# Performance work log

Hardware: AMD Instinct MI355X
Metric: run time of the kernel (lower is better)

Reference implementation:

```python
import jax, jax.numpy as jnp
import numpy as np

NEG_SLOPE = 0.2


def gat_layer(x, src, dst, W, a_src, a_dst, bias, num_nodes, concat):
    """PyG-style GATConv (eval mode, self-loops already included in src/dst).
    x: [N, F_in]; W: [F_in, H*C]; a_src, a_dst: [H, C]; bias: [H*C] or [C].
    """
    H, C = a_src.shape
    h = (x @ W).reshape(num_nodes, H, C)                    # [N,H,C]
    alpha_s = jnp.einsum('nhc,hc->nh', h, a_src)            # [N,H]
    alpha_d = jnp.einsum('nhc,hc->nh', h, a_dst)            # [N,H]
    e = alpha_s[src] + alpha_d[dst]                         # [E,H]
    e = jnp.where(e > 0, e, NEG_SLOPE * e)                  # LeakyReLU(0.2)
    # segment softmax over destination nodes (numerically stable)
    m = jax.ops.segment_max(e, dst, num_segments=num_nodes)  # [N,H]
    m = jnp.where(jnp.isfinite(m), m, 0.0)
    ex = jnp.exp(e - m[dst])                                # [E,H]
    s = jax.ops.segment_sum(ex, dst, num_segments=num_nodes)  # [N,H]
    alpha = ex / (s[dst] + 1e-16)                           # [E,H]
    msg = h[src] * alpha[:, :, None]                        # [E,H,C]
    out = jax.ops.segment_sum(msg, dst, num_segments=num_nodes)  # [N,H,C]
    if concat:
        out = out.reshape(num_nodes, H * C)
    else:
        out = out.mean(axis=1)
    return out + bias


def _forward(x, edge_index, W1, a_src1, a_dst1, b1, W2, a_src2, a_dst2, b2):
    N = x.shape[0]
    loops = jnp.arange(N, dtype=edge_index.dtype)
    src = jnp.concatenate([edge_index[0], loops])
    dst = jnp.concatenate([edge_index[1], loops])
    h = gat_layer(x, src, dst, W1, a_src1, a_dst1, b1, N, concat=True)
    h = jax.nn.relu(h)  # dropout inactive in eval
    h = gat_layer(h, src, dst, W2, a_src2, a_dst2, b2, N, concat=False)
    return jax.nn.log_softmax(h, axis=1)


def setup_inputs() -> dict:
    key = jax.random.key(0)
    ks = jax.random.split(key, 10)
    N, E, F_in, Hid, H1, F_out = 100000, 1600000, 128, 64, 2, 7
    x = jax.random.normal(ks[0], (N, F_in), dtype=jnp.float32)
    edge_index = jax.random.randint(ks[1], (2, E), 0, N, dtype=jnp.int64)
    s1 = 1.0 / np.sqrt(F_in)
    W1 = jax.random.uniform(ks[2], (F_in, H1 * Hid), jnp.float32, -s1, s1)
    a_src1 = jax.random.uniform(ks[3], (H1, Hid), jnp.float32, -s1, s1)
    a_dst1 = jax.random.uniform(ks[4], (H1, Hid), jnp.float32, -s1, s1)
    b1 = jnp.zeros((H1 * Hid,), jnp.float32)
    s2 = 1.0 / np.sqrt(H1 * Hid)
    W2 = jax.random.uniform(ks[5], (H1 * Hid, F_out), jnp.float32, -s2, s2)
    a_src2 = jax.random.uniform(ks[6], (1, F_out), jnp.float32, -s2, s2)
    a_dst2 = jax.random.uniform(ks[7], (1, F_out), jnp.float32, -s2, s2)
    b2 = jnp.zeros((F_out,), jnp.float32)
    return {"x": x, "edge_index": edge_index, "W1": W1, "a_src1": a_src1,
            "a_dst1": a_dst1, "b1": b1, "W2": W2, "a_src2": a_src2,
            "a_dst2": a_dst2, "b2": b2}


def reference(x, edge_index, W1, a_src1, a_dst1, b1, W2, a_src2, a_dst2, b2):
    return _forward(x, edge_index, W1, a_src1, a_dst1, b1, W2, a_src2, a_dst2, b2)
```

## Files before the change

### kernel.cpp

```cpp
#include <hip/hip_runtime.h>
#include <hip/hip_bf16.h>

#define F_IN 128
#define HC   128
#define C1   64
#define F_OUT 7
#define H2S  8
#define BSH  9
#define BSZ  512
#define BINCH 4096
#define BCAP 12288

typedef __attribute__((ext_vector_type(8))) short short8;
typedef __attribute__((ext_vector_type(4))) float f32x4;
typedef __attribute__((ext_vector_type(2))) float f32x2;

__device__ __forceinline__ ushort f2bf(float f) {
    uint u = __builtin_bit_cast(uint, f);
    u = (u + 0x7FFFu + ((u >> 16) & 1u)) >> 16;
    return (ushort)u;
}

__device__ __forceinline__ int perm_col(int p_byte) {
    int slp = p_byte >> 3, j = p_byte & 7;
    int h = slp >> 3, sg = slp & 7;
    int lr = 2 * sg + (j >> 2), jj = j & 3;
    return 16 * (4 * h + jj) + lr;
}

__global__ __launch_bounds__(256) void k_cvt(
    const float* __restrict__ W1, ushort* __restrict__ Wsw,
    const float* __restrict__ W2, const float* __restrict__ b1,
    float* __restrict__ W2p, float* __restrict__ b1p, int* __restrict__ bcnt)
{
    int b = blockIdx.x, t = threadIdx.x;
    if (b < 64) {
        int i = b * 256 + t;
        int k = i >> 7, n = i & 127;
        float v = W1[k * HC + n];
        int idx = n * 128 + (((k & ~7) ^ ((n & 7) << 3)) | (k & 7));
        Wsw[idx] = f2bf(v);
    } else {
        bcnt[t] = 0;
        for (int i = t; i < 128 * F_OUT; i += 256) {
            int p = i / F_OUT, o = i - p * F_OUT;
            W2p[i] = W2[perm_col(p) * F_OUT + o];
        }
        if (t < 128) b1p[t] = b1[perm_col(t)];
    }
}

__global__ __launch_bounds__(256) void k_bingemm(
    const int* __restrict__ ei, int E, int Etot, int NBIN,
    int* __restrict__ bcnt, uint* __restrict__ binned,
    const float* __restrict__ x, const ushort* __restrict__ Wsw,
    const float* __restrict__ a_src, const float* __restrict__ a_dst,
    unsigned char* __restrict__ h1p, float* __restrict__ as1, float* __restrict__ ad1,
    int N)
{
    __shared__ __align__(16) char smem[128 * 128 * 2];
    const int t = threadIdx.x;

    if ((int)blockIdx.x < NBIN) {
        int* hist = (int*)smem;
        int* base = hist + 256;
        hist[t] = 0;
        __syncthreads();
        long c0 = (long)blockIdx.x * BINCH;
        uint val[16]; int bkt[16];
#pragma unroll
        for (int i2 = 0; i2 < 16; ++i2) {
            long e = c0 + t + i2 * 256;
            int s = 0, d = 0;
            bkt[i2] = -1;
            if (e < Etot) {
                if (e < E) { s = ei[e]; d = ei[E + e]; } else { s = (int)(e - E); d = s; }
                bkt[i2] = d >> BSH;
                atomicAdd(&hist[bkt[i2]], 1);
            }
            val[i2] = ((uint)s << BSH) | (uint)(d & (BSZ - 1));
        }
        __syncthreads();
        base[t] = t * BCAP + ((hist[t] > 0) ? atomicAdd(&bcnt[t], hist[t]) : 0);
        __syncthreads();
#pragma unroll
        for (int i2 = 0; i2 < 16; ++i2) {
            if (bkt[i2] >= 0) {
                int pos = atomicAdd(&base[bkt[i2]], 1);
                if (pos < (bkt[i2] + 1) * BCAP)
                    binned[pos] = val[i2];
            }
        }
    } else {
        ushort* Bs = (ushort*)smem;
        const int w = t >> 6, l = t & 63;
        const int lr = l & 15, hi = l >> 4;
        const int n0 = (blockIdx.x - NBIN) * 64;

        {
            const uint4* src = (const uint4*)Wsw;
            uint4* dst = (uint4*)Bs;
#pragma unroll
            for (int it = 0; it < 8; ++it) dst[t + it * 256] = src[t + it * 256];
        }
        __syncthreads();

        f32x4 acc[8];
#pragma unroll
        for (int j = 0; j < 8; ++j) acc[j] = (f32x4){0.f, 0.f, 0.f, 0.f};

        int arow = n0 + w * 16 + lr;
        if (arow >= N) arow = N - 1;
        const float* aptr = x + (size_t)arow * F_IN + hi * 8;

#pragma unroll
        for (int kt = 0; kt < 4; ++kt) {
            float4 f0 = *(const float4*)(aptr + kt * 32);
            float4 f1 = *(const float4*)(aptr + kt * 32 + 4);
            short8 a;
            a[0] = (short)f2bf(f0.x); a[1] = (short)f2bf(f0.y);
            a[2] = (short)f2bf(f0.z); a[3] = (short)f2bf(f0.w);
            a[4] = (short)f2bf(f1.x); a[5] = (short)f2bf(f1.y);
            a[6] = (short)f2bf(f1.z); a[7] = (short)f2bf(f1.w);
#pragma unroll
            for (int j = 0; j < 8; ++j) {
                int rn = 16 * j + lr;
                int kidx = (kt * 32 + hi * 8) ^ ((rn & 7) << 3);
                short8 b = *(const short8*)(Bs + rn * 128 + kidx);
                acc[j] = __builtin_amdgcn_mfma_f32_16x16x32_bf16(a, b, acc[j], 0, 0, 0);
            }
        }

        float as_[8], ad_[8];
#pragma unroll
        for (int j = 0; j < 8; ++j) {
            int hd = j >> 2;
            int c = 16 * (j & 3) + lr;
            as_[j] = a_src[hd * C1 + c];
            ad_[j] = a_dst[hd * C1 + c];
        }
#pragma unroll
        for (int i = 0; i < 4; ++i) {
            int r = n0 + w * 16 + hi * 4 + i;
            float ps0 = 0, ps1 = 0, pd0 = 0, pd1 = 0;
#pragma unroll
            for (int j = 0; j < 4; ++j) { ps0 += acc[j][i] * as_[j]; pd0 += acc[j][i] * ad_[j]; }
#pragma unroll
            for (int j = 4; j < 8; ++j) { ps1 += acc[j][i] * as_[j]; pd1 += acc[j][i] * ad_[j]; }
#pragma unroll
            for (int off = 1; off <= 8; off <<= 1) {
                ps0 += __shfl_xor(ps0, off, 64);
                ps1 += __shfl_xor(ps1, off, 64);
                pd0 += __shfl_xor(pd0, off, 64);
                pd1 += __shfl_xor(pd1, off, 64);
            }
            if (r < N) {
                int w0 = 0, w1 = 0;
                w0 = __builtin_amdgcn_cvt_pk_fp8_f32(acc[0][i], acc[1][i], w0, false);
                w0 = __builtin_amdgcn_cvt_pk_fp8_f32(acc[2][i], acc[3][i], w0, true);
                w1 = __builtin_amdgcn_cvt_pk_fp8_f32(acc[4][i], acc[5][i], w1, false);
                w1 = __builtin_amdgcn_cvt_pk_fp8_f32(acc[6][i], acc[7][i], w1, true);
                *(uint*)(h1p + (size_t)r * HC + lr * 4)      = (uint)w0;
                *(uint*)(h1p + (size_t)r * HC + 64 + lr * 4) = (uint)w1;
                if (lr == 0) {
                    as1[r * 2 + 0] = ps0; as1[r * 2 + 1] = ps1;
                    ad1[r * 2 + 0] = pd0; ad1[r * 2 + 1] = pd1;
                }
            }
        }
    }
}

__global__ __launch_bounds__(256) void k_fill(
    const uint* __restrict__ binned, const int* __restrict__ bcnt,
    int* __restrict__ rowptr, int* __restrict__ csr, int N, int NB)
{
    __shared__ int deg[BSZ];
    __shared__ int cur[BSZ];
    __shared__ int sc[256];
    int b = blockIdx.x, t = threadIdx.x;
    int cv = (t < NB) ? min(bcnt[t], BCAP) : 0;
    sc[t] = cv;
    __syncthreads();
    for (int off = 1; off < 256; off <<= 1) {
        int u = (t >= off) ? sc[t - off] : 0;
        __syncthreads();
        sc[t] += u;
        __syncthreads();
    }
    int total = sc[255];
    int s0 = (b > 0) ? sc[b - 1] : 0;
    int cntb = min(bcnt[b], BCAP);
    __syncthreads();

    int n0 = b << BSH;
    int nn = N - n0; if (nn > BSZ) nn = BSZ;
    deg[t] = 0; deg[t + 256] = 0;
    __syncthreads();
    const uint* bb = binned + (size_t)b * BCAP;
    for (int i = t; i < cntb; i += 256)
        atomicAdd(&deg[bb[i] & (BSZ - 1)], 1);
    __syncthreads();
    int d0 = deg[2 * t], d1 = deg[2 * t + 1];
    int ts = d0 + d1;
    sc[t] = ts;
    __syncthreads();
    for (int off = 1; off < 256; off <<= 1) {
        int u = (t >= off) ? sc[t - off] : 0;
        __syncthreads();
        sc[t] += u;
        __syncthreads();
    }
    int ex = sc[t] - ts + s0;
    if (2 * t < nn)     { rowptr[n0 + 2 * t]     = ex;      cur[2 * t]     = ex; }
    if (2 * t + 1 < nn) { rowptr[n0 + 2 * t + 1] = ex + d0; cur[2 * t + 1] = ex + d0; }
    __syncthreads();
    for (int i = t; i < cntb; i += 256) {
        uint en = bb[i];
        int pos = atomicAdd(&cur[en & (BSZ - 1)], 1);
        csr[pos] = (int)(en >> BSH);
    }
    if (b == 0 && t == 0) rowptr[N] = total;
}

__global__ __launch_bounds__(256) void k_aggr1_l2(
    const int* __restrict__ rowptr, const int* __restrict__ csr_src,
    const float* __restrict__ as1, const float* __restrict__ ad1,
    const unsigned char* __restrict__ h1p, const float* __restrict__ b1p,
    const float* __restrict__ W2p, const float* __restrict__ a_src2,
    const float* __restrict__ a_dst2,
    float* __restrict__ h2p, float* __restrict__ ad2,
    int N)
{
    int w = threadIdx.x >> 6, l = threadIdx.x & 63;
    int q = l >> 4, sl = l & 15;
    int n = blockIdx.x * 16 + w * 4 + q;
    if (n >= N) return;
    const int h = sl >> 3;
    const int boff = sl * 8;
    float adv = ad1[n * 2 + h];
    int beg = rowptr[n], end = rowptr[n + 1];
    f32x2 ac01 = {0.f, 0.f}, ac23 = {0.f, 0.f}, ac45 = {0.f, 0.f}, ac67 = {0.f, 0.f};
    float s = 0.f;

    int i = beg;
    for (; i + 4 <= end; i += 4) {
        int sv[4]; float Av[4]; uint2 Hv[4];
#pragma unroll
        for (int j = 0; j < 4; ++j) sv[j] = csr_src[i + j];
#pragma unroll
        for (int j = 0; j < 4; ++j) Av[j] = as1[sv[j] * 2 + h];
#pragma unroll
        for (int j = 0; j < 4; ++j)
            Hv[j] = *(const uint2*)(h1p + (((size_t)(uint)sv[j]) << 7) + boff);
#pragma unroll
        for (int j = 0; j < 4; ++j) {
            float a = Av[j] + adv; a = a > 0.f ? a : 0.2f * a;
            float e = __expf(a);
            s += e;
            f32x2 ev = {e, e};
            ac01 += ev * __builtin_amdgcn_cvt_pk_f32_fp8((int)Hv[j].x, false);
            ac23 += ev * __builtin_amdgcn_cvt_pk_f32_fp8((int)Hv[j].x, true);
            ac45 += ev * __builtin_amdgcn_cvt_pk_f32_fp8((int)Hv[j].y, false);
            ac67 += ev * __builtin_amdgcn_cvt_pk_f32_fp8((int)Hv[j].y, true);
        }
    }
    for (; i < end; ++i) {
        int src = csr_src[i];
        float a = as1[src * 2 + h] + adv; a = a > 0.f ? a : 0.2f * a;
        float e = __expf(a);
        s += e;
        uint2 hv = *(const uint2*)(h1p + (((size_t)(uint)src) << 7) + boff);
        f32x2 ev = {e, e};
        ac01 += ev * __builtin_amdgcn_cvt_pk_f32_fp8((int)hv.x, false);
        ac23 += ev * __builtin_amdgcn_cvt_pk_f32_fp8((int)hv.x, true);
        ac45 += ev * __builtin_amdgcn_cvt_pk_f32_fp8((int)hv.y, false);
        ac67 += ev * __builtin_amdgcn_cvt_pk_f32_fp8((int)hv.y, true);
    }
    float inv = 1.f / (s + 1e-16f);

    float4 bv0 = *(const float4*)&b1p[sl * 8];
    float4 bv1 = *(const float4*)&b1p[sl * 8 + 4];
    float v[8];
    v[0] = fmaxf(ac01[0] * inv + bv0.x, 0.f);
    v[1] = fmaxf(ac01[1] * inv + bv0.y, 0.f);
    v[2] = fmaxf(ac23[0] * inv + bv0.z, 0.f);
    v[3] = fmaxf(ac23[1] * inv + bv0.w, 0.f);
    v[4] = fmaxf(ac45[0] * inv + bv1.x, 0.f);
    v[5] = fmaxf(ac45[1] * inv + bv1.y, 0.f);
    v[6] = fmaxf(ac67[0] * inv + bv1.z, 0.f);
    v[7] = fmaxf(ac67[1] * inv + bv1.w, 0.f);

    float w2r[56];
    {
        const float4* wp = (const float4*)(W2p + sl * 56);
#pragma unroll
        for (int k = 0; k < 14; ++k) {
            float4 f = wp[k];
            w2r[4 * k + 0] = f.x; w2r[4 * k + 1] = f.y;
            w2r[4 * k + 2] = f.z; w2r[4 * k + 3] = f.w;
        }
    }
    float p[7];
#pragma unroll
    for (int j = 0; j < 7; ++j) p[j] = 0.f;
#pragma unroll
    for (int r = 0; r < 8; ++r)
#pragma unroll
        for (int j = 0; j < 7; ++j) p[j] += v[r] * w2r[r * 7 + j];
#pragma unroll
    for (int off = 1; off <= 8; off <<= 1)
#pragma unroll
        for (int j = 0; j < 7; ++j) p[j] += __shfl_xor(p[j], off, 64);

    if (sl == 0) {
        float asv = 0.f, adv2 = 0.f;
#pragma unroll
        for (int j = 0; j < 7; ++j) {
            h2p[(size_t)n * H2S + j] = p[j];
            asv += p[j] * a_src2[j];
            adv2 += p[j] * a_dst2[j];
        }
        h2p[(size_t)n * H2S + 7] = asv;
        ad2[n] = adv2;
    }
}

__global__ __launch_bounds__(256) void k_aggr2ls(
    const int* __restrict__ rowptr, const int* __restrict__ csr_src,
    const float* __restrict__ ad2,
    const float* __restrict__ h2p, const float* __restrict__ b2,
    float* __restrict__ out, int N)
{
    int g = blockIdx.x * blockDim.x + threadIdx.x;
    int n = g >> 2, l = g & 2 | (g & 1);
    l = g & 3;
    if (n >= N) return;
    float adv = ad2[n];
    int beg = rowptr[n], end = rowptr[n + 1];
    f32x2 acc = {0.f, 0.f};
    float s = 0.f;
    int i = beg;
    for (; i + 4 <= end; i += 4) {
        int sv[4]; float2 Hv[4];
#pragma unroll
        for (int j = 0; j < 4; ++j) sv[j] = csr_src[i + j];
#pragma unroll
        for (int j = 0; j < 4; ++j)
            Hv[j] = *(const float2*)(h2p + ((size_t)(uint)sv[j]) * H2S + 2 * l);
#pragma unroll
        for (int j = 0; j < 4; ++j) {
            float as2v = __shfl(Hv[j].y, 3, 4);
            float a = as2v + adv;
            a = a > 0.f ? a : 0.2f * a;
            float e = __expf(a);
            s += e;
            f32x2 ev = {e, e};
            f32x2 hv = {Hv[j].x, Hv[j].y};
            acc += ev * hv;
        }
    }
    for (; i < end; ++i) {
        int s0 = csr_src[i];
        float2 hv2 = *(const float2*)(h2p + ((size_t)(uint)s0) * H2S + 2 * l);
        float as2v = __shfl(hv2.y, 3, 4);
        float a = as2v + adv;
        a = a > 0.f ? a : 0.2f * a;
        float e = __expf(a);
        s += e;
        f32x2 ev = {e, e};
        f32x2 hv = {hv2.x, hv2.y};
        acc += ev * hv;
    }
    float invs = 1.f / (s + 1e-16f);
    float va = acc[0] * invs + b2[2 * l];
    float vb = (2 * l + 1 < 7) ? acc[1] * invs + b2[2 * l + 1] : -1e30f;
    float m = fmaxf(va, vb);
#pragma unroll
    for (int off = 1; off <= 2; off <<= 1)
        m = fmaxf(m, __shfl_xor(m, off, 4));
    float ex = __expf(va - m) + ((2 * l + 1 < 7) ? __expf(vb - m) : 0.f);
#pragma unroll
    for (int off = 1; off <= 2; off <<= 1)
        ex += __shfl_xor(ex, off, 4);
    float lg = __logf(ex);
    out[(size_t)n * F_OUT + 2 * l] = va - m - lg;
    if (2 * l + 1 < 7) out[(size_t)n * F_OUT + 2 * l + 1] = vb - m - lg;
}

extern "C" void kernel_launch(void* const* d_in, const int* in_sizes, int n_in,
                              void* d_out, int out_size, void* d_ws, size_t ws_size,
                              hipStream_t stream) {
    const float* x      = (const float*)d_in[0];
    const int*   ei     = (const int*)d_in[1];
    const float* W1     = (const float*)d_in[2];
    const float* a_src1 = (const float*)d_in[3];
    const float* a_dst1 = (const float*)d_in[4];
    const float* b1     = (const float*)d_in[5];
    const float* W2     = (const float*)d_in[6];
    const float* a_src2 = (const float*)d_in[7];
    const float* a_dst2 = (const float*)d_in[8];
    const float* b2     = (const float*)d_in[9];
    float* out = (float*)d_out;

    const int N    = in_sizes[0] / F_IN;
    const int E    = in_sizes[1] / 2;
    const int Etot = E + N;
    const int NB   = (N + BSZ - 1) >> BSH;
    const int NBIN = (Etot + BINCH - 1) / BINCH;

    char* ws = (char*)d_ws;
    size_t off = 0;
    auto A = [&](size_t bytes) -> void* {
        char* p = ws + off;
        off += (bytes + 255) & ~(size_t)255;
        return (void*)p;
    };
    ushort* Wsw    = (ushort*)A((size_t)128 * 128 * 2);
    float*  W2p    = (float*) A((size_t)128 * F_OUT * 4);
    float*  b1p    = (float*) A((size_t)128 * 4);
    unsigned char* h1p = (unsigned char*)A((size_t)N * HC);
    float*  as1    = (float*) A((size_t)N * 2 * 4);
    float*  ad1    = (float*) A((size_t)N * 2 * 4);
    int*    rowptr = (int*)   A((size_t)(N + 1) * 4);
    int*    csr    = (int*)   A((size_t)Etot * 4);
    int*    bcnt   = (int*)   A(256 * 4);
    uint*   binned = (uint*)  A((size_t)NB * BCAP * 4);
    float*  h2p    = (float*)binned;
    float*  ad2    = (float*)((char*)binned + (((size_t)N * H2S * 4 + 255) & ~(size_t)255));

    k_cvt<<<65, 256, 0, stream>>>(W1, Wsw, W2, b1, W2p, b1p, bcnt);
    k_bingemm<<<NBIN + (N + 63) / 64, 256, 0, stream>>>(
        ei, E, Etot, NBIN, bcnt, binned,
        x, Wsw, a_src1, a_dst1, h1p, as1, ad1, N);
    k_fill<<<NB, 256, 0, stream>>>(binned, bcnt, rowptr, csr, N, NB);
    k_aggr1_l2<<<(N + 15) / 16, 256, 0, stream>>>(rowptr, csr, as1, ad1, h1p,
                                                  b1p, W2p, a_src2, a_dst2,
                                                  h2p, ad2, N);
    k_aggr2ls<<<((size_t)N * 4 + 255) / 256, 256, 0, stream>>>(rowptr, csr,
                                                               ad2, h2p, b2, out, N);
}
```

Measured before the change: 134.6 us.

## Remove weight-conversion kernel by folding W1 conversion into GEMM and W2 permute into fill

Drops the separate k_cvt launch. Each GEMM block now converts W1 to bf16 and writes it swizzled straight into shared memory, the W2/b1 permutation runs in an extra block of k_fill, and bcnt is zeroed with a memset. The aggregation kernels also prefetch the next group of CSR source indices one iteration ahead. This trades one launch for redundant W1 reads and conversion in every GEMM block (about 1563 blocks, each doing strided global loads), which could cost more than the launch it removes.

```diff
diff --git a/kernel.cpp b/kernel.cpp
--- a/kernel.cpp
+++ b/kernel.cpp
@@ -28,32 +28,10 @@
     return 16 * (4 * h + jj) + lr;
 }
 
-__global__ __launch_bounds__(256) void k_cvt(
-    const float* __restrict__ W1, ushort* __restrict__ Wsw,
-    const float* __restrict__ W2, const float* __restrict__ b1,
-    float* __restrict__ W2p, float* __restrict__ b1p, int* __restrict__ bcnt)
-{
-    int b = blockIdx.x, t = threadIdx.x;
-    if (b < 64) {
-        int i = b * 256 + t;
-        int k = i >> 7, n = i & 127;
-        float v = W1[k * HC + n];
-        int idx = n * 128 + (((k & ~7) ^ ((n & 7) << 3)) | (k & 7));
-        Wsw[idx] = f2bf(v);
-    } else {
-        bcnt[t] = 0;
-        for (int i = t; i < 128 * F_OUT; i += 256) {
-            int p = i / F_OUT, o = i - p * F_OUT;
-            W2p[i] = W2[perm_col(p) * F_OUT + o];
-        }
-        if (t < 128) b1p[t] = b1[perm_col(t)];
-    }
-}
-
 __global__ __launch_bounds__(256) void k_bingemm(
     const int* __restrict__ ei, int E, int Etot, int NBIN,
     int* __restrict__ bcnt, uint* __restrict__ binned,
-    const float* __restrict__ x, const ushort* __restrict__ Wsw,
+    const float* __restrict__ x, const float* __restrict__ W1,
     const float* __restrict__ a_src, const float* __restrict__ a_dst,
     unsigned char* __restrict__ h1p, float* __restrict__ as1, float* __restrict__ ad1,
     int N)
@@ -98,10 +76,15 @@
         const int n0 = (blockIdx.x - NBIN) * 64;
 
         {
-            const uint4* src = (const uint4*)Wsw;
-            uint4* dst = (uint4*)Bs;
-#pragma unroll
-            for (int it = 0; it < 8; ++it) dst[t + it * 256] = src[t + it * 256];
+            int n = t & 127;
+            int k0 = (t >> 7) * 64;
+#pragma unroll
+            for (int j = 0; j < 64; ++j) {
+                int k = k0 + j;
+                float v = W1[k * HC + n];
+                int dst = n * 128 + (((k & ~7) ^ ((n & 7) << 3)) | (k & 7));
+                Bs[dst] = f2bf(v);
+            }
         }
         __syncthreads();
 
@@ -173,12 +156,23 @@
 
 __global__ __launch_bounds__(256) void k_fill(
     const uint* __restrict__ binned, const int* __restrict__ bcnt,
-    int* __restrict__ rowptr, int* __restrict__ csr, int N, int NB)
+    int* __restrict__ rowptr, int* __restrict__ csr,
+    const float* __restrict__ W2, const float* __restrict__ b1,
+    float* __restrict__ W2p, float* __restrict__ b1p,
+    int N, int NB)
 {
+    int b = blockIdx.x, t = threadIdx.x;
+    if (b == NB) {
+        for (int i = t; i < 128 * F_OUT; i += 256) {
+            int p = i / F_OUT, o = i - p * F_OUT;
+            W2p[i] = W2[perm_col(p) * F_OUT + o];
+        }
+        if (t < 128) b1p[t] = b1[perm_col(t)];
+        return;
+    }
     __shared__ int deg[BSZ];
     __shared__ int cur[BSZ];
     __shared__ int sc[256];
-    int b = blockIdx.x, t = threadIdx.x;
     int cv = (t < NB) ? min(bcnt[t], BCAP) : 0;
     sc[t] = cv;
     __syncthreads();
@@ -244,15 +238,25 @@
     float s = 0.f;
 
     int i = beg;
+    int sv[4];
+    if (i + 4 <= end) {
+#pragma unroll
+        for (int j = 0; j < 4; ++j) sv[j] = csr_src[i + j];
+    }
     for (; i + 4 <= end; i += 4) {
-        int sv[4]; float Av[4]; uint2 Hv[4];
-#pragma unroll
-        for (int j = 0; j < 4; ++j) sv[j] = csr_src[i + j];
-#pragma unroll
-        for (int j = 0; j < 4; ++j) Av[j] = as1[sv[j] * 2 + h];
+        int cv[4];
+#pragma unroll
+        for (int j = 0; j < 4; ++j) cv[j] = sv[j];
+        if (i + 8 <= end) {
+#pragma unroll
+            for (int j = 0; j < 4; ++j) sv[j] = csr_src[i + 4 + j];
+        }
+        float Av[4]; uint2 Hv[4];
+#pragma unroll
+        for (int j = 0; j < 4; ++j) Av[j] = as1[cv[j] * 2 + h];
 #pragma unroll
         for (int j = 0; j < 4; ++j)
-            Hv[j] = *(const uint2*)(h1p + (((size_t)(uint)sv[j]) << 7) + boff);
+            Hv[j] = *(const uint2*)(h1p + (((size_t)(uint)cv[j]) << 7) + boff);
 #pragma unroll
         for (int j = 0; j < 4; ++j) {
             float a = Av[j] + adv; a = a > 0.f ? a : 0.2f * a;
@@ -333,21 +337,30 @@
     float* __restrict__ out, int N)
 {
     int g = blockIdx.x * blockDim.x + threadIdx.x;
-    int n = g >> 2, l = g & 2 | (g & 1);
-    l = g & 3;
+    int n = g >> 2, l = g & 3;
     if (n >= N) return;
     float adv = ad2[n];
     int beg = rowptr[n], end = rowptr[n + 1];
     f32x2 acc = {0.f, 0.f};
     float s = 0.f;
     int i = beg;
+    int sv[4];
+    if (i + 4 <= end) {
+#pragma unroll
+        for (int j = 0; j < 4; ++j) sv[j] = csr_src[i + j];
+    }
     for (; i + 4 <= end; i += 4) {
-        int sv[4]; float2 Hv[4];
-#pragma unroll
-        for (int j = 0; j < 4; ++j) sv[j] = csr_src[i + j];
+        int cv[4];
+#pragma unroll
+        for (int j = 0; j < 4; ++j) cv[j] = sv[j];
+        if (i + 8 <= end) {
+#pragma unroll
+            for (int j = 0; j < 4; ++j) sv[j] = csr_src[i + 4 + j];
+        }
+        float2 Hv[4];
 #pragma unroll
         for (int j = 0; j < 4; ++j)
-            Hv[j] = *(const float2*)(h2p + ((size_t)(uint)sv[j]) * H2S + 2 * l);
+            Hv[j] = *(const float2*)(h2p + ((size_t)(uint)cv[j]) * H2S + 2 * l);
 #pragma unroll
         for (int j = 0; j < 4; ++j) {
             float as2v = __shfl(Hv[j].y, 3, 4);
@@ -416,7 +429,6 @@
         off += (bytes + 255) & ~(size_t)255;
         return (void*)p;
     };
-    ushort* Wsw    = (ushort*)A((size_t)128 * 128 * 2);
     float*  W2p    = (float*) A((size_t)128 * F_OUT * 4);
     float*  b1p    = (float*) A((size_t)128 * 4);
     unsigned char* h1p = (unsigned char*)A((size_t)N * HC);
@@ -429,11 +441,13 @@
     float*  h2p    = (float*)binned;
     float*  ad2    = (float*)((char*)binned + (((size_t)N * H2S * 4 + 255) & ~(size_t)255));
 
-    k_cvt<<<65, 256, 0, stream>>>(W1, Wsw, W2, b1, W2p, b1p, bcnt);
+    hipMemsetAsync(bcnt, 0, 256 * 4, stream);
+
     k_bingemm<<<NBIN + (N + 63) / 64, 256, 0, stream>>>(
         ei, E, Etot, NBIN, bcnt, binned,
-        x, Wsw, a_src1, a_dst1, h1p, as1, ad1, N);
-    k_fill<<<NB, 256, 0, stream>>>(binned, bcnt, rowptr, csr, N, NB);
+        x, W1, a_src1, a_dst1, h1p, as1, ad1, N);
+    k_fill<<<NB + 1, 256, 0, stream>>>(binned, bcnt, rowptr, csr,
+                                       W2, b1, W2p, b1p, N, NB);
     k_aggr1_l2<<<(N + 15) / 16, 256, 0, stream>>>(rowptr, csr, as1, ad1, h1p,
                                                   b1p, W2p, a_src2, a_dst2,
                                                   h2p, ad2, N);
```

Measured after the change: 134.6 us. About the same (+0.1%).
